# Performance work log

Measured on AMD Instinct MI355X. Metric: run time of the kernel, lower is better.

## Reference

```python
import jax, jax.numpy as jnp
import numpy as np

D_MODEL = 1024
NUM_HEADS = 16
D_K = D_MODEL // NUM_HEADS
B, S = 2, 2048


def setup_inputs() -> dict:
    key = jax.random.key(0)
    ks = jax.random.split(key, 13)
    s = 1.0 / np.sqrt(D_MODEL)
    inp = {
        "query": jax.random.normal(ks[0], (B, S, D_MODEL), jnp.float32),
        "key_": jax.random.normal(ks[1], (B, S, D_MODEL), jnp.float32),
        "value": jax.random.normal(ks[2], (B, S, D_MODEL), jnp.float32),
        "mask": jax.random.randint(ks[3], (B, 1, 1, S), 0, 2, jnp.int32),
        # torch nn.Linear convention: weight (out, in), y = x @ W.T + b
        "Wq": jax.random.uniform(ks[4], (D_MODEL, D_MODEL), jnp.float32, -s, s),
        "bq": jax.random.uniform(ks[5], (D_MODEL,), jnp.float32, -s, s),
        "Wk": jax.random.uniform(ks[6], (D_MODEL, D_MODEL), jnp.float32, -s, s),
        "bk": jax.random.uniform(ks[7], (D_MODEL,), jnp.float32, -s, s),
        "Wv": jax.random.uniform(ks[8], (D_MODEL, D_MODEL), jnp.float32, -s, s),
        "bv": jax.random.uniform(ks[9], (D_MODEL,), jnp.float32, -s, s),
        "Wo": jax.random.uniform(ks[10], (D_MODEL, D_MODEL), jnp.float32, -s, s),
        "bo": jax.random.uniform(ks[11], (D_MODEL,), jnp.float32, -s, s),
    }
    return inp


def _split_heads(x):
    b, s, _ = x.shape
    return x.reshape(b, s, NUM_HEADS, D_K).transpose(0, 2, 1, 3)  # (B,H,S,dk)


def reference(query, key_, value, mask, Wq, bq, Wk, bk, Wv, bv, Wo, bo):
    Q = _split_heads(query @ Wq.T + bq)
    K = _split_heads(key_ @ Wk.T + bk)
    V = _split_heads(value @ Wv.T + bv)
    scores = jnp.einsum("bhqd,bhkd->bhqk", Q, K) / np.sqrt(D_K).astype(np.float32)
    scores = jnp.where(mask == 0, -jnp.inf, scores)
    attn = jax.nn.softmax(scores, axis=-1)
    attn = jnp.nan_to_num(attn)  # fully-masked rows -> 0 (matches torch.nan_to_num)
    ctx = jnp.einsum("bhqk,bhkd->bhqd", attn, V)
    concat = ctx.transpose(0, 2, 1, 3).reshape(query.shape[0], -1, D_MODEL)
    out = concat @ Wo.T + bo  # dropout is identity in eval mode
    return out
```

## Files before the change

kernel.cpp:

```cpp
#include <hip/hip_runtime.h>
#include <math.h>

#define D_MODEL 1024
#define NUM_HEADS 16
#define DK 64
#define BATCH 2
#define SEQ 2048

using f32x4  = __attribute__((ext_vector_type(4))) float;
using f16x8  = __attribute__((ext_vector_type(8))) _Float16;

__device__ __forceinline__ void gl_lds16(const void* g, void* l) {
    __builtin_amdgcn_global_load_lds(
        (const __attribute__((address_space(1))) void*)g,
        (__attribute__((address_space(3))) void*)l, 16, 0, 0);
}

__global__ __launch_bounds__(256) void mask_scan_kernel(
    const int* __restrict__ mask, int* __restrict__ pos, int* __restrict__ nc)
{
    const int b = blockIdx.x;
    const int tid = threadIdx.x;
    __shared__ int sums[256];
    int v[8]; int cnt = 0;
    const int base = b * SEQ + tid * 8;
    #pragma unroll
    for (int e = 0; e < 8; ++e) { v[e] = (mask[base + e] != 0) ? 1 : 0; cnt += v[e]; }
    sums[tid] = cnt;
    __syncthreads();
    for (int off = 1; off < 256; off <<= 1) {
        int t = (tid >= off) ? sums[tid - off] : 0;
        __syncthreads();
        sums[tid] += t;
        __syncthreads();
    }
    int run = sums[tid] - cnt;
    #pragma unroll
    for (int e = 0; e < 8; ++e) { pos[base + e] = run; run += v[e]; }
    if (tid == 255) nc[b] = sums[255];
}

__global__ __launch_bounds__(256) void conv_all_kernel(
    const float* Wq, const float* Wk, const float* Wv, const float* Wo,
    const float* query, const float* key_, const float* value,
    _Float16* w2q, _Float16* w2k, _Float16* w2v, _Float16* w2o,
    _Float16* aq, _Float16* ak, _Float16* av,
    const int* __restrict__ mask, const int* __restrict__ pos)
{
    const int y = blockIdx.y;
    const float* src; _Float16* dst; int rows; bool compact = false;
    switch (y) {
        case 0: src = Wq;    dst = w2q; rows = 1024; break;
        case 1: src = Wk;    dst = w2k; rows = 1024; break;
        case 2: src = Wv;    dst = w2v; rows = 1024; break;
        case 3: src = Wo;    dst = w2o; rows = 1024; break;
        case 4: src = query; dst = aq;  rows = 4096; break;
        case 5: src = key_;  dst = ak;  rows = 4096; compact = true; break;
        default: src = value; dst = av; rows = 4096; compact = true; break;
    }
    const int id = blockIdx.x * 256 + threadIdx.x;
    if (id >= rows * 128) return;
    const int row = id >> 7;
    int drow = row;
    if (compact) {
        if (!mask[row]) return;
        drow = (row >> 11) * SEQ + pos[row];
    }
    const int s  = id & 127;
    const int g  = s >> 3, ss = s & 7;
    const int lb = ss ^ (drow & 7);

    const float* p = src + (size_t)row * 1024 + g * 64 + lb * 8;
    const float4 a = *(const float4*)p;
    const float4 bq = *(const float4*)(p + 4);
    f16x8 o;
    o[0] = (_Float16)a.x;  o[1] = (_Float16)a.y;
    o[2] = (_Float16)a.z;  o[3] = (_Float16)a.w;
    o[4] = (_Float16)bq.x; o[5] = (_Float16)bq.y;
    o[6] = (_Float16)bq.z; o[7] = (_Float16)bq.w;
    *(f16x8*)&dst[(size_t)drow * 1024 + s * 8] = o;
}

template <int MODE>
__global__ __launch_bounds__(256) void mfma_gemm_f16_kernel(
    const _Float16* __restrict__ A2, const _Float16* __restrict__ W2,
    const float* __restrict__ bias, float* __restrict__ Cf,
    _Float16* __restrict__ Ch, const int* __restrict__ ncArr)
{
    constexpr int KS = 1024;
    __shared__ f16x8 Asl[3][1024];
    __shared__ f16x8 Bsl[3][512];

    const int bm = blockIdx.x * 128, bn = blockIdx.y * 64;
    if (MODE == 2 || MODE == 3) {
        if ((bm & (SEQ - 1)) >= ncArr[bm >> 11]) return;
    }

    const int tid = threadIdx.x;
    const int wv = tid >> 6, ln = tid & 63;
    const int wm = wv >> 1, wn = wv & 1;
    const int x = ln & 15, y = ln >> 4;

    f32x4 acc[4][2] = {};

    const _Float16* Ab = A2 + (size_t)bm * KS;
    const _Float16* Bb = W2 + (size_t)bn * KS;
    const int srow = ln >> 3;
    const int scol = (ln & 7) * 8;

    auto stage = [&](int bufi, int kt) {
        #pragma unroll
        for (int c = 0; c < 4; ++c) {
            const int rowb = wv * 32 + c * 8;
            gl_lds16(Ab + (size_t)(rowb + srow) * KS + kt * 64 + scol,
                     &Asl[bufi][rowb << 3]);
        }
        #pragma unroll
        for (int c = 0; c < 2; ++c) {
            const int rowb = wv * 16 + c * 8;
            gl_lds16(Bb + (size_t)(rowb + srow) * KS + kt * 64 + scol,
                     &Bsl[bufi][rowb << 3]);
        }
    };

    stage(0, 0);
    stage(1, 1);

    int buf = 0, sbuf = 2;
    for (int kt = 0; kt < 16; ++kt) {
        if (kt < 15) asm volatile("s_waitcnt vmcnt(6)" ::: "memory");
        else         asm volatile("s_waitcnt vmcnt(0)" ::: "memory");
        __builtin_amdgcn_s_barrier();
        if (kt + 2 < 16) stage(sbuf, kt + 2);
        #pragma unroll
        for (int half = 0; half < 2; ++half) {
            f16x8 af[4], bfr[2];
            #pragma unroll
            for (int mf = 0; mf < 4; ++mf) {
                const int r = wm * 64 + mf * 16 + x;
                af[mf] = Asl[buf][(r << 3) | ((half * 4 + y) ^ (r & 7))];
            }
            #pragma unroll
            for (int nf = 0; nf < 2; ++nf) {
                const int r = wn * 32 + nf * 16 + x;
                bfr[nf] = Bsl[buf][(r << 3) | ((half * 4 + y) ^ (r & 7))];
            }
            #pragma unroll
            for (int mf = 0; mf < 4; ++mf)
                #pragma unroll
                for (int nf = 0; nf < 2; ++nf)
                    acc[mf][nf] = __builtin_amdgcn_mfma_f32_16x16x32_f16(
                        af[mf], bfr[nf], acc[mf][nf], 0, 0, 0);
        }
        buf  = (buf  == 2) ? 0 : buf  + 1;
        sbuf = (sbuf == 2) ? 0 : sbuf + 1;
    }

    #pragma unroll
    for (int nf = 0; nf < 2; ++nf) {
        const int n = bn + wn * 32 + nf * 16 + x;
        const float bv = bias[n];
        #pragma unroll
        for (int mf = 0; mf < 4; ++mf) {
            const int mbase = bm + wm * 64 + mf * 16 + y * 4;
            #pragma unroll
            for (int r = 0; r < 4; ++r) {
                const int m = mbase + r;
                const float v = acc[mf][nf][r] + bv;
                const int b = m >> 11, s = m & (SEQ - 1);
                const int hh = n >> 6, dd = n & 63;
                if (MODE == 0) {
                    Cf[(size_t)m * D_MODEL + n] = v;
                } else if (MODE == 1) {
                    const int blk = (dd >> 3) ^ (s & 7), i = dd & 7;
                    Ch[((size_t)((b * NUM_HEADS + hh) * SEQ + s)) * 64 +
                       blk * 8 + i] = (_Float16)(v * 0.125f);
                } else if (MODE == 2) {
                    if (s < ncArr[b]) {
                        const int blk = (dd >> 3) ^ (s & 7), i = dd & 7;
                        Ch[((size_t)((b * NUM_HEADS + hh) * SEQ + s)) * 64 +
                           blk * 8 + i] = (_Float16)v;
                    }
                } else {
                    if (s < ncArr[b]) {
                        const int tile = s >> 6, w = s & 63;
                        const int blk = (w >> 3) ^ (dd & 7), i = w & 7;
                        Ch[((size_t)((b * NUM_HEADS + hh) * DK + dd)) * SEQ +
                           tile * 64 + blk * 8 + i] = (_Float16)v;
                    }
                }
            }
        }
    }
}

__global__ __launch_bounds__(256, 4) void attn_mfma_kernel(
    const _Float16* __restrict__ Q2, const _Float16* __restrict__ K2,
    const _Float16* __restrict__ VT2, const int* __restrict__ ncArr,
    _Float16* __restrict__ ACT)
{
    __shared__ __align__(16) _Float16 SM[20480];

    const int tid = threadIdx.x;
    const int wave = tid >> 6, lane = tid & 63;
    const int lo4 = lane & 15, hi4 = lane >> 4;
    _Float16* Pw = SM + 16384 + wave * 1024;

    const int orig = blockIdx.x;
    const int swz = (orig & 7) * 128 + (orig >> 3);
    const int bh = swz >> 5, qblk = swz & 31;
    const int b = bh >> 4, h = bh & 15;

    const _Float16* Kb = K2 + (size_t)bh * SEQ * 64;
    const _Float16* Vb = VT2 + (size_t)bh * DK * SEQ;

    const int ncb = ncArr[b];
    const int ntiles = (ncb + 63) >> 6;

    const int qr = qblk * 64 + wave * 16 + lo4;
    const _Float16* Q2row = Q2 + (size_t)(bh * SEQ + qr) * 64;
    f16x8 qf[2];
    #pragma unroll
    for (int c = 0; c < 2; ++c)
        qf[c] = *(const f16x8*)&Q2row[(((c * 4 + hi4) ^ (qr & 7)) * 8)];

    auto stage_kv = [&](int base, int k0) {
        #pragma unroll
        for (int j = 0; j < 4; ++j) {
            const int g = j * 256 + wave * 64;
            const int gi = g + lane;
            const _Float16* src;
            if (gi < 512) {
                src = Kb + (size_t)(k0 + (gi >> 3)) * 64 + (gi & 7) * 8;
            } else {
                const int g2 = gi - 512;
                src = Vb + (size_t)(g2 >> 3) * SEQ + k0 + (g2 & 7) * 8;
            }
            gl_lds16(src, SM + base + (size_t)g * 8);
        }
    };

    f32x4 ctx[4] = {};
    float m = -INFINITY, l = 0.f;

    stage_kv(0, 0);
    for (int t = 0; t < ntiles; ++t) {
        if (t + 1 < ntiles) {
            stage_kv(((t + 1) & 1) * 8192, (t + 1) * 64);
            asm volatile("s_waitcnt vmcnt(4)" ::: "memory");
        } else {
            asm volatile("s_waitcnt vmcnt(0)" ::: "memory");
        }
        __builtin_amdgcn_s_barrier();

        const _Float16* Ks = SM + (t & 1) * 8192;
        const _Float16* VTs = Ks + 4096;
        const int k0 = t * 64;

        f32x4 sc[4];
        __builtin_amdgcn_s_setprio(1);
        #pragma unroll
        for (int kt = 0; kt < 4; ++kt) {
            f32x4 s = {0.f, 0.f, 0.f, 0.f};
            const int row = kt * 16 + lo4;
            const int rx = row & 7;
            #pragma unroll
            for (int c = 0; c < 2; ++c) {
                const f16x8 kf = *(f16x8*)&Ks[row * 64 + (((c * 4 + hi4) ^ rx) * 8)];
                s = __builtin_amdgcn_mfma_f32_16x16x32_f16(kf, qf[c], s, 0, 0, 0);
            }
            sc[kt] = s;
        }
        __builtin_amdgcn_s_setprio(0);

        float cmax = -1e30f;
        if (k0 + 64 <= ncb) {
            #pragma unroll
            for (int kt = 0; kt < 4; ++kt)
                #pragma unroll
                for (int r = 0; r < 4; ++r) cmax = fmaxf(cmax, sc[kt][r]);
        } else {
            #pragma unroll
            for (int kt = 0; kt < 4; ++kt)
                #pragma unroll
                for (int r = 0; r < 4; ++r) {
                    const int kidx = k0 + kt * 16 + hi4 * 4 + r;
                    const float sv = (kidx < ncb) ? sc[kt][r] : -1e30f;
                    sc[kt][r] = sv;
                    cmax = fmaxf(cmax, sv);
                }
        }
        cmax = fmaxf(cmax, __shfl_xor(cmax, 16));
        cmax = fmaxf(cmax, __shfl_xor(cmax, 32));

        const bool grow = __any(cmax > m);
        const float mold = m;
        const float mnew = grow ? fmaxf(m, cmax) : m;
        m = mnew;

        float ps = 0.f;
        #pragma unroll
        for (int kt = 0; kt < 4; ++kt) {
            const float pv0 = __expf(sc[kt][0] - mnew);
            const float pv1 = __expf(sc[kt][1] - mnew);
            const float pv2 = __expf(sc[kt][2] - mnew);
            const float pv3 = __expf(sc[kt][3] - mnew);
            ps += (pv0 + pv1) + (pv2 + pv3);
            union { _Float16 hh[2]; unsigned u; } pk0, pk1;
            pk0.hh[0] = (_Float16)pv0; pk0.hh[1] = (_Float16)pv1;
            pk1.hh[0] = (_Float16)pv2; pk1.hh[1] = (_Float16)pv3;
            const int blk16 = (kt * 2 + (hi4 >> 1)) ^ (lo4 & 7);
            unsigned* dst = (unsigned*)&Pw[lo4 * 64 + blk16 * 8 + (hi4 & 1) * 4];
            dst[0] = pk0.u; dst[1] = pk1.u;
        }
        ps += __shfl_xor(ps, 16);
        ps += __shfl_xor(ps, 32);

        if (grow) {
            const float e1 = __expf(mold - mnew);
            l = l * e1 + ps;
            #pragma unroll
            for (int dt = 0; dt < 4; ++dt)
                #pragma unroll
                for (int r = 0; r < 4; ++r) ctx[dt][r] *= e1;
        } else {
            l += ps;
        }

        __builtin_amdgcn_s_setprio(1);
        #pragma unroll
        for (int c = 0; c < 2; ++c) {
            const f16x8 pf = *(f16x8*)&Pw[lo4 * 64 + (((c * 4 + hi4) ^ (lo4 & 7)) * 8)];
            #pragma unroll
            for (int dt = 0; dt < 4; ++dt) {
                const int row = dt * 16 + lo4;
                const f16x8 vf =
                    *(f16x8*)&VTs[row * 64 + (((c * 4 + hi4) ^ (row & 7)) * 8)];
                ctx[dt] = __builtin_amdgcn_mfma_f32_16x16x32_f16(vf, pf, ctx[dt], 0, 0, 0);
            }
        }
        __builtin_amdgcn_s_setprio(0);

        __builtin_amdgcn_s_barrier();
    }

    __syncthreads();
    const float inv = (l > 0.f) ? (1.f / l) : 0.f;
    float* OutL = (float*)SM;
    #pragma unroll
    for (int dt = 0; dt < 4; ++dt)
        #pragma unroll
        for (int r = 0; r < 4; ++r)
            OutL[(wave * 16 + lo4) * 68 + dt * 16 + hi4 * 4 + r] = ctx[dt][r] * inv;
    __syncthreads();
    {
        const int row = tid >> 2, cb = (tid & 3) * 16;
        const int mrow = b * SEQ + qblk * 64 + row;
        _Float16* arow = ACT + (size_t)mrow * 1024;
        #pragma unroll
        for (int u = 0; u < 2; ++u) {
            const int lb = (cb >> 3) + u;
            const int ss = lb ^ (mrow & 7);
            f16x8 hv;
            #pragma unroll
            for (int i = 0; i < 8; ++i)
                hv[i] = (_Float16)OutL[row * 68 + cb + u * 8 + i];
            *(f16x8*)&arow[h * 64 + ss * 8] = hv;
        }
    }
}

template <int SPLIT>
__global__ __launch_bounds__(256) void gemm_bias_kernel(
    const float* __restrict__ A, const float* __restrict__ W,
    const float* __restrict__ bias, float* __restrict__ C,
    int M, int N, int K)
{
    constexpr int TILE = 64, KT = 16;
    __shared__ float As[KT][TILE + 4];
    __shared__ float Ws[KT][TILE + 4];
    const int tid = threadIdx.x;
    const int tx = tid & 15, ty = tid >> 4;
    const int bm = blockIdx.x * TILE, bn = blockIdx.y * TILE;
    const int lrow = tid >> 2, lk4 = (tid & 3) << 2;
    float acc[4][4] = {{0.f}};
    for (int k0 = 0; k0 < K; k0 += KT) {
        const float4 a4 = *(const float4*)&A[(size_t)(bm + lrow) * K + k0 + lk4];
        const float4 w4 = *(const float4*)&W[(size_t)(bn + lrow) * K + k0 + lk4];
        __syncthreads();
        As[lk4 + 0][lrow] = a4.x; As[lk4 + 1][lrow] = a4.y;
        As[lk4 + 2][lrow] = a4.z; As[lk4 + 3][lrow] = a4.w;
        Ws[lk4 + 0][lrow] = w4.x; Ws[lk4 + 1][lrow] = w4.y;
        Ws[lk4 + 2][lrow] = w4.z; Ws[lk4 + 3][lrow] = w4.w;
        __syncthreads();
        #pragma unroll
        for (int kk = 0; kk < KT; ++kk) {
            const float4 av = *(const float4*)&As[kk][ty << 2];
            const float4 wv = *(const float4*)&Ws[kk][tx << 2];
            acc[0][0] += av.x * wv.x; acc[0][1] += av.x * wv.y; acc[0][2] += av.x * wv.z; acc[0][3] += av.x * wv.w;
            acc[1][0] += av.y * wv.x; acc[1][1] += av.y * wv.y; acc[1][2] += av.y * wv.z; acc[1][3] += av.y * wv.w;
            acc[2][0] += av.z * wv.x; acc[2][1] += av.z * wv.y; acc[2][2] += av.z * wv.z; acc[2][3] += av.z * wv.w;
            acc[3][0] += av.w * wv.x; acc[3][1] += av.w * wv.y; acc[3][2] += av.w * wv.z; acc[3][3] += av.w * wv.w;
        }
    }
    const float4 bb = *(const float4*)&bias[bn + (tx << 2)];
    #pragma unroll
    for (int i = 0; i < 4; ++i) {
        const int row = bm + (ty << 2) + i;
        float4 o;
        o.x = acc[i][0] + bb.x; o.y = acc[i][1] + bb.y;
        o.z = acc[i][2] + bb.z; o.w = acc[i][3] + bb.w;
        if (SPLIT) {
            const int b = row >> 11, s = row & (SEQ - 1), hh = bn >> 6;
            *(float4*)&C[((size_t)((b * NUM_HEADS + hh) * SEQ + s)) * DK + (tx << 2)] = o;
        } else {
            *(float4*)&C[(size_t)row * N + bn + (tx << 2)] = o;
        }
    }
}

__global__ __launch_bounds__(256, 2) void attn_fp32_kernel(
    const float* __restrict__ Q, const float* __restrict__ K,
    const float* __restrict__ V, const int* __restrict__ mask,
    float* __restrict__ OUT)
{
    const int qb = blockIdx.x, h = blockIdx.y, b = blockIdx.z;
    const int wave = threadIdx.x >> 6, lane = threadIdx.x & 63;
    const int tid = threadIdx.x;
    const int bh = b * NUM_HEADS + h;
    const float* Qb = Q + (size_t)bh * SEQ * DK;
    const float* Kb = K + (size_t)bh * SEQ * DK;
    const float* Vb = V + (size_t)bh * SEQ * DK;
    const int* mb = mask + b * SEQ;
    __shared__ float Ks[64][68];
    __shared__ float Vs[64][68];
    const int row = qb * 256 + wave * 64 + lane;
    float q[DK], ctx[DK];
    #pragma unroll
    for (int d4 = 0; d4 < 16; ++d4) {
        const float4 t = *(const float4*)&Qb[(size_t)row * DK + 4 * d4];
        q[4*d4] = t.x; q[4*d4+1] = t.y; q[4*d4+2] = t.z; q[4*d4+3] = t.w;
        ctx[4*d4] = 0.f; ctx[4*d4+1] = 0.f; ctx[4*d4+2] = 0.f; ctx[4*d4+3] = 0.f;
    }
    float m = -INFINITY, l = 0.f;
    for (int t = 0; t < SEQ / 64; ++t) {
        const int k0 = t * 64;
        const float* Kt = Kb + (size_t)k0 * DK;
        const float* Vt = Vb + (size_t)k0 * DK;
        __syncthreads();
        #pragma unroll
        for (int i = 0; i < 4; ++i) {
            const int f4 = i * 256 + tid;
            const int r = f4 >> 4, c = (f4 & 15) << 2;
            *(float4*)&Ks[r][c] = *(const float4*)&Kt[4 * f4];
            *(float4*)&Vs[r][c] = *(const float4*)&Vt[4 * f4];
        }
        __syncthreads();
        const unsigned long long mbits = __ballot(mb[k0 + lane] != 0);
        if (mbits == 0ULL) continue;
        for (int c0 = 0; c0 < 64; c0 += 16) {
            const unsigned bits = (unsigned)((mbits >> c0) & 0xFFFFULL);
            if (!bits) continue;
            float sc[16];
            #pragma unroll
            for (int j = 0; j < 16; ++j) {
                if (!((bits >> j) & 1u)) { sc[j] = -INFINITY; continue; }
                float a0 = 0.f, a1 = 0.f, a2 = 0.f, a3 = 0.f;
                #pragma unroll
                for (int d4 = 0; d4 < 16; ++d4) {
                    const float4 kv = *(const float4*)&Ks[c0 + j][4 * d4];
                    a0 += q[4*d4] * kv.x; a1 += q[4*d4+1] * kv.y;
                    a2 += q[4*d4+2] * kv.z; a3 += q[4*d4+3] * kv.w;
                }
                sc[j] = ((a0 + a1) + (a2 + a3)) * 0.125f;
            }
            float cmax = sc[0];
            #pragma unroll
            for (int j = 1; j < 16; ++j) cmax = fmaxf(cmax, sc[j]);
            if (cmax > m) {
                const float scale = __expf(m - cmax);
                l *= scale;
                #pragma unroll
                for (int d = 0; d < DK; ++d) ctx[d] *= scale;
                m = cmax;
            }
            #pragma unroll
            for (int j = 0; j < 16; ++j) {
                if (!((bits >> j) & 1u)) continue;
                const float p = __expf(sc[j] - m);
                l += p;
                #pragma unroll
                for (int d4 = 0; d4 < 16; ++d4) {
                    const float4 vv = *(const float4*)&Vs[c0 + j][4 * d4];
                    ctx[4*d4] += p * vv.x; ctx[4*d4+1] += p * vv.y;
                    ctx[4*d4+2] += p * vv.z; ctx[4*d4+3] += p * vv.w;
                }
            }
        }
    }
    const float inv = (l > 0.f) ? (1.f / l) : 0.f;
    float* dst = OUT + ((size_t)(b * SEQ + row)) * D_MODEL + h * DK;
    #pragma unroll
    for (int d4 = 0; d4 < 16; ++d4) {
        float4 o;
        o.x = ctx[4*d4] * inv; o.y = ctx[4*d4+1] * inv;
        o.z = ctx[4*d4+2] * inv; o.w = ctx[4*d4+3] * inv;
        *(float4*)&dst[4 * d4] = o;
    }
}

extern "C" void kernel_launch(void* const* d_in, const int* in_sizes, int n_in,
                              void* d_out, int out_size, void* d_ws, size_t ws_size,
                              hipStream_t stream)
{
    const float* query = (const float*)d_in[0];
    const float* key_  = (const float*)d_in[1];
    const float* value = (const float*)d_in[2];
    const int*   mask  = (const int*)d_in[3];
    const float* Wq = (const float*)d_in[4];
    const float* bq = (const float*)d_in[5];
    const float* Wk = (const float*)d_in[6];
    const float* bk = (const float*)d_in[7];
    const float* Wv = (const float*)d_in[8];
    const float* bv = (const float*)d_in[9];
    const float* Wo = (const float*)d_in[10];
    const float* bo = (const float*)d_in[11];
    float* out = (float*)d_out;

    const int M = BATCH * SEQ;
    const size_t ACT_B = (size_t)M * 1024 * 2;
    const size_t W_B   = (size_t)D_MODEL * 1024 * 2;
    const size_t K2_B  = (size_t)32 * SEQ * 64 * 2;
    const size_t VT2_B = (size_t)32 * DK * SEQ * 2;
    const size_t Q2_B  = K2_B;
    const size_t POS_B = (size_t)BATCH * SEQ * 4 + 256;

    char* base = (char*)d_ws;
    _Float16* actQh = (_Float16*)(base);
    _Float16* actKh = (_Float16*)(base + ACT_B);
    _Float16* actVh = (_Float16*)(base + 2 * ACT_B);
    _Float16* actO  = (_Float16*)(base + 3 * ACT_B);
    _Float16* w2qh  = (_Float16*)(base + 4 * ACT_B);
    _Float16* w2kh  = (_Float16*)((char*)w2qh + W_B);
    _Float16* w2vh  = (_Float16*)((char*)w2kh + W_B);
    _Float16* w2oh  = (_Float16*)((char*)w2vh + W_B);
    _Float16* k2    = (_Float16*)((char*)w2oh + W_B);
    _Float16* vt2   = (_Float16*)((char*)k2 + K2_B);
    _Float16* q2    = (_Float16*)((char*)vt2 + VT2_B);
    int* posArr = (int*)((char*)q2 + Q2_B);
    int* ncArr  = posArr + BATCH * SEQ;
    const size_t need = 4 * ACT_B + 4 * W_B + K2_B + VT2_B + Q2_B + POS_B;

    if (ws_size >= need) {
        mask_scan_kernel<<<BATCH, 256, 0, stream>>>(mask, posArr, ncArr);

        conv_all_kernel<<<dim3(2048, 7), 256, 0, stream>>>(
            Wq, Wk, Wv, Wo, query, key_, value,
            w2qh, w2kh, w2vh, w2oh, actQh, actKh, actVh, mask, posArr);

        dim3 ggrid(M / 128, D_MODEL / 64);
        mfma_gemm_f16_kernel<2><<<ggrid, 256, 0, stream>>>(
            actKh, w2kh, bk, nullptr, k2, ncArr);
        mfma_gemm_f16_kernel<3><<<ggrid, 256, 0, stream>>>(
            actVh, w2vh, bv, nullptr, vt2, ncArr);
        mfma_gemm_f16_kernel<1><<<ggrid, 256, 0, stream>>>(
            actQh, w2qh, bq, nullptr, q2, ncArr);

        attn_mfma_kernel<<<1024, 256, 0, stream>>>(q2, k2, vt2, ncArr, actO);

        mfma_gemm_f16_kernel<0><<<ggrid, 256, 0, stream>>>(
            actO, w2oh, bo, out, nullptr, ncArr);
    } else {
        float* q_ws = (float*)(base);
        float* k_ws = (float*)(base + (size_t)M * D_MODEL * 4);
        float* v_ws = (float*)(base + 2 * (size_t)M * D_MODEL * 4);
        float* c_ws = (float*)(base + 3 * (size_t)M * D_MODEL * 4);
        dim3 ggrid(M / 64, D_MODEL / 64);
        gemm_bias_kernel<1><<<ggrid, 256, 0, stream>>>(query, Wq, bq, q_ws, M, D_MODEL, D_MODEL);
        gemm_bias_kernel<1><<<ggrid, 256, 0, stream>>>(key_,  Wk, bk, k_ws, M, D_MODEL, D_MODEL);
        gemm_bias_kernel<1><<<ggrid, 256, 0, stream>>>(value, Wv, bv, v_ws, M, D_MODEL, D_MODEL);
        dim3 agrid(SEQ / 256, NUM_HEADS, BATCH);
        attn_fp32_kernel<<<agrid, 256, 0, stream>>>(q_ws, k_ws, v_ws, mask, c_ws);
        gemm_bias_kernel<0><<<ggrid, 256, 0, stream>>>(c_ws, Wo, bo, out, M, D_MODEL, D_MODEL);
    }
}
```

Measured before the change: 130.7 us.

## Process 128 query rows per attention block to reuse staged K/V tiles

Each wave now handles two 16-row query fragments instead of one, so every block covers 128 query rows and the grid halves from 1024 to 512 blocks. Each K/V tile staged into LDS is reused for twice as many queries, which halves global K/V traffic and the barrier count per query. In exchange, register pressure rises (two context accumulators and two sets of softmax state), the occupancy hint in launch_bounds is dropped, and fewer blocks are available to fill the GPU's compute units.

```diff
diff --git a/kernel.cpp b/kernel.cpp
--- a/kernel.cpp
+++ b/kernel.cpp
@@ -194,7 +194,7 @@
     }
 }
 
-__global__ __launch_bounds__(256, 4) void attn_mfma_kernel(
+__global__ __launch_bounds__(256) void attn_mfma_kernel(
     const _Float16* __restrict__ Q2, const _Float16* __restrict__ K2,
     const _Float16* __restrict__ VT2, const int* __restrict__ ncArr,
     _Float16* __restrict__ ACT)
@@ -207,8 +207,8 @@
     _Float16* Pw = SM + 16384 + wave * 1024;
 
     const int orig = blockIdx.x;
-    const int swz = (orig & 7) * 128 + (orig >> 3);
-    const int bh = swz >> 5, qblk = swz & 31;
+    const int swz = (orig & 7) * 64 + (orig >> 3);
+    const int bh = swz >> 4, qblk = swz & 15;
     const int b = bh >> 4, h = bh & 15;
 
     const _Float16* Kb = K2 + (size_t)bh * SEQ * 64;
@@ -217,12 +217,15 @@
     const int ncb = ncArr[b];
     const int ntiles = (ncb + 63) >> 6;
 
-    const int qr = qblk * 64 + wave * 16 + lo4;
-    const _Float16* Q2row = Q2 + (size_t)(bh * SEQ + qr) * 64;
-    f16x8 qf[2];
-    #pragma unroll
-    for (int c = 0; c < 2; ++c)
-        qf[c] = *(const f16x8*)&Q2row[(((c * 4 + hi4) ^ (qr & 7)) * 8)];
+    f16x8 qf[2][2];
+    #pragma unroll
+    for (int f = 0; f < 2; ++f) {
+        const int qr = qblk * 128 + wave * 32 + f * 16 + lo4;
+        const _Float16* Q2row = Q2 + (size_t)(bh * SEQ + qr) * 64;
+        #pragma unroll
+        for (int c = 0; c < 2; ++c)
+            qf[f][c] = *(const f16x8*)&Q2row[(((c * 4 + hi4) ^ (qr & 7)) * 8)];
+    }
 
     auto stage_kv = [&](int base, int k0) {
         #pragma unroll
@@ -240,8 +243,8 @@
         }
     };
 
-    f32x4 ctx[4] = {};
-    float m = -INFINITY, l = 0.f;
+    f32x4 ctx[2][4] = {};
+    float m[2] = {-INFINITY, -INFINITY}, l[2] = {0.f, 0.f};
 
     stage_kv(0, 0);
     for (int t = 0; t < ntiles; ++t) {
@@ -256,116 +259,125 @@
         const _Float16* Ks = SM + (t & 1) * 8192;
         const _Float16* VTs = Ks + 4096;
         const int k0 = t * 64;
-
-        f32x4 sc[4];
-        __builtin_amdgcn_s_setprio(1);
-        #pragma unroll
-        for (int kt = 0; kt < 4; ++kt) {
-            f32x4 s = {0.f, 0.f, 0.f, 0.f};
-            const int row = kt * 16 + lo4;
-            const int rx = row & 7;
+        const bool fulltile = (k0 + 64 <= ncb);
+
+        #pragma unroll
+        for (int f = 0; f < 2; ++f) {
+            f32x4 sc[4];
+            __builtin_amdgcn_s_setprio(1);
+            #pragma unroll
+            for (int kt = 0; kt < 4; ++kt) {
+                f32x4 s = {0.f, 0.f, 0.f, 0.f};
+                const int row = kt * 16 + lo4;
+                const int rx = row & 7;
+                #pragma unroll
+                for (int c = 0; c < 2; ++c) {
+                    const f16x8 kf = *(f16x8*)&Ks[row * 64 + (((c * 4 + hi4) ^ rx) * 8)];
+                    s = __builtin_amdgcn_mfma_f32_16x16x32_f16(kf, qf[f][c], s, 0, 0, 0);
+                }
+                sc[kt] = s;
+            }
+            __builtin_amdgcn_s_setprio(0);
+
+            float cmax = -1e30f;
+            if (fulltile) {
+                #pragma unroll
+                for (int kt = 0; kt < 4; ++kt)
+                    #pragma unroll
+                    for (int r = 0; r < 4; ++r) cmax = fmaxf(cmax, sc[kt][r]);
+            } else {
+                #pragma unroll
+                for (int kt = 0; kt < 4; ++kt)
+                    #pragma unroll
+                    for (int r = 0; r < 4; ++r) {
+                        const int kidx = k0 + kt * 16 + hi4 * 4 + r;
+                        const float sv = (kidx < ncb) ? sc[kt][r] : -1e30f;
+                        sc[kt][r] = sv;
+                        cmax = fmaxf(cmax, sv);
+                    }
+            }
+            cmax = fmaxf(cmax, __shfl_xor(cmax, 16));
+            cmax = fmaxf(cmax, __shfl_xor(cmax, 32));
+
+            const bool grow = __any(cmax > m[f]);
+            const float mold = m[f];
+            const float mnew = grow ? fmaxf(m[f], cmax) : m[f];
+            m[f] = mnew;
+
+            float ps = 0.f;
+            #pragma unroll
+            for (int kt = 0; kt < 4; ++kt) {
+                const float pv0 = __expf(sc[kt][0] - mnew);
+                const float pv1 = __expf(sc[kt][1] - mnew);
+                const float pv2 = __expf(sc[kt][2] - mnew);
+                const float pv3 = __expf(sc[kt][3] - mnew);
+                ps += (pv0 + pv1) + (pv2 + pv3);
+                union { _Float16 hh[2]; unsigned u; } pk0, pk1;
+                pk0.hh[0] = (_Float16)pv0; pk0.hh[1] = (_Float16)pv1;
+                pk1.hh[0] = (_Float16)pv2; pk1.hh[1] = (_Float16)pv3;
+                const int blk16 = (kt * 2 + (hi4 >> 1)) ^ (lo4 & 7);
+                unsigned* dst = (unsigned*)&Pw[lo4 * 64 + blk16 * 8 + (hi4 & 1) * 4];
+                dst[0] = pk0.u; dst[1] = pk1.u;
+            }
+            ps += __shfl_xor(ps, 16);
+            ps += __shfl_xor(ps, 32);
+
+            if (grow) {
+                const float e1 = __expf(mold - mnew);
+                l[f] = l[f] * e1 + ps;
+                #pragma unroll
+                for (int dt = 0; dt < 4; ++dt)
+                    #pragma unroll
+                    for (int r = 0; r < 4; ++r) ctx[f][dt][r] *= e1;
+            } else {
+                l[f] += ps;
+            }
+
+            __builtin_amdgcn_s_setprio(1);
             #pragma unroll
             for (int c = 0; c < 2; ++c) {
-                const f16x8 kf = *(f16x8*)&Ks[row * 64 + (((c * 4 + hi4) ^ rx) * 8)];
-                s = __builtin_amdgcn_mfma_f32_16x16x32_f16(kf, qf[c], s, 0, 0, 0);
-            }
-            sc[kt] = s;
-        }
-        __builtin_amdgcn_s_setprio(0);
-
-        float cmax = -1e30f;
-        if (k0 + 64 <= ncb) {
-            #pragma unroll
-            for (int kt = 0; kt < 4; ++kt)
-                #pragma unroll
-                for (int r = 0; r < 4; ++r) cmax = fmaxf(cmax, sc[kt][r]);
-        } else {
-            #pragma unroll
-            for (int kt = 0; kt < 4; ++kt)
-                #pragma unroll
-                for (int r = 0; r < 4; ++r) {
-                    const int kidx = k0 + kt * 16 + hi4 * 4 + r;
-                    const float sv = (kidx < ncb) ? sc[kt][r] : -1e30f;
-                    sc[kt][r] = sv;
-                    cmax = fmaxf(cmax, sv);
+                const f16x8 pf = *(f16x8*)&Pw[lo4 * 64 + (((c * 4 + hi4) ^ (lo4 & 7)) * 8)];
+                #pragma unroll
+                for (int dt = 0; dt < 4; ++dt) {
+                    const int row = dt * 16 + lo4;
+                    const f16x8 vf =
+                        *(f16x8*)&VTs[row * 64 + (((c * 4 + hi4) ^ (row & 7)) * 8)];
+                    ctx[f][dt] = __builtin_amdgcn_mfma_f32_16x16x32_f16(vf, pf, ctx[f][dt], 0, 0, 0);
                 }
-        }
-        cmax = fmaxf(cmax, __shfl_xor(cmax, 16));
-        cmax = fmaxf(cmax, __shfl_xor(cmax, 32));
-
-        const bool grow = __any(cmax > m);
-        const float mold = m;
-        const float mnew = grow ? fmaxf(m, cmax) : m;
-        m = mnew;
-
-        float ps = 0.f;
-        #pragma unroll
-        for (int kt = 0; kt < 4; ++kt) {
-            const float pv0 = __expf(sc[kt][0] - mnew);
-            const float pv1 = __expf(sc[kt][1] - mnew);
-            const float pv2 = __expf(sc[kt][2] - mnew);
-            const float pv3 = __expf(sc[kt][3] - mnew);
-            ps += (pv0 + pv1) + (pv2 + pv3);
-            union { _Float16 hh[2]; unsigned u; } pk0, pk1;
-            pk0.hh[0] = (_Float16)pv0; pk0.hh[1] = (_Float16)pv1;
-            pk1.hh[0] = (_Float16)pv2; pk1.hh[1] = (_Float16)pv3;
-            const int blk16 = (kt * 2 + (hi4 >> 1)) ^ (lo4 & 7);
-            unsigned* dst = (unsigned*)&Pw[lo4 * 64 + blk16 * 8 + (hi4 & 1) * 4];
-            dst[0] = pk0.u; dst[1] = pk1.u;
-        }
-        ps += __shfl_xor(ps, 16);
-        ps += __shfl_xor(ps, 32);
-
-        if (grow) {
-            const float e1 = __expf(mold - mnew);
-            l = l * e1 + ps;
-            #pragma unroll
-            for (int dt = 0; dt < 4; ++dt)
-                #pragma unroll
-                for (int r = 0; r < 4; ++r) ctx[dt][r] *= e1;
-        } else {
-            l += ps;
-        }
-
-        __builtin_amdgcn_s_setprio(1);
-        #pragma unroll
-        for (int c = 0; c < 2; ++c) {
-            const f16x8 pf = *(f16x8*)&Pw[lo4 * 64 + (((c * 4 + hi4) ^ (lo4 & 7)) * 8)];
-            #pragma unroll
-            for (int dt = 0; dt < 4; ++dt) {
-                const int row = dt * 16 + lo4;
-                const f16x8 vf =
-                    *(f16x8*)&VTs[row * 64 + (((c * 4 + hi4) ^ (row & 7)) * 8)];
-                ctx[dt] = __builtin_amdgcn_mfma_f32_16x16x32_f16(vf, pf, ctx[dt], 0, 0, 0);
-            }
-        }
-        __builtin_amdgcn_s_setprio(0);
+            }
+            __builtin_amdgcn_s_setprio(0);
+        }
 
         __builtin_amdgcn_s_barrier();
     }
 
-    __syncthreads();
-    const float inv = (l > 0.f) ? (1.f / l) : 0.f;
-    float* OutL = (float*)SM;
-    #pragma unroll
-    for (int dt = 0; dt < 4; ++dt)
-        #pragma unroll
-        for (int r = 0; r < 4; ++r)
-            OutL[(wave * 16 + lo4) * 68 + dt * 16 + hi4 * 4 + r] = ctx[dt][r] * inv;
-    __syncthreads();
-    {
-        const int row = tid >> 2, cb = (tid & 3) * 16;
-        const int mrow = b * SEQ + qblk * 64 + row;
-        _Float16* arow = ACT + (size_t)mrow * 1024;
-        #pragma unroll
-        for (int u = 0; u < 2; ++u) {
-            const int lb = (cb >> 3) + u;
-            const int ss = lb ^ (mrow & 7);
-            f16x8 hv;
-            #pragma unroll
-            for (int i = 0; i < 8; ++i)
-                hv[i] = (_Float16)OutL[row * 68 + cb + u * 8 + i];
-            *(f16x8*)&arow[h * 64 + ss * 8] = hv;
+    #pragma unroll
+    for (int f = 0; f < 2; ++f) {
+        __syncthreads();
+        const float inv = (l[f] > 0.f) ? (1.f / l[f]) : 0.f;
+        float* OutL = (float*)SM;
+        #pragma unroll
+        for (int dt = 0; dt < 4; ++dt)
+            #pragma unroll
+            for (int r = 0; r < 4; ++r)
+                OutL[(wave * 16 + lo4) * 68 + dt * 16 + hi4 * 4 + r] =
+                    ctx[f][dt][r] * inv;
+        __syncthreads();
+        {
+            const int row = tid >> 2, cb = (tid & 3) * 16;
+            const int mrow = b * SEQ + qblk * 128 + (row >> 4) * 32 + f * 16
+                           + (row & 15);
+            _Float16* arow = ACT + (size_t)mrow * 1024;
+            #pragma unroll
+            for (int u = 0; u < 2; ++u) {
+                const int lb = (cb >> 3) + u;
+                const int ss = lb ^ (mrow & 7);
+                f16x8 hv;
+                #pragma unroll
+                for (int i = 0; i < 8; ++i)
+                    hv[i] = (_Float16)OutL[row * 68 + cb + u * 8 + i];
+                *(f16x8*)&arow[h * 64 + ss * 8] = hv;
+            }
         }
     }
 }
@@ -566,7 +578,7 @@
         mfma_gemm_f16_kernel<1><<<ggrid, 256, 0, stream>>>(
             actQh, w2qh, bq, nullptr, q2, ncArr);
 
-        attn_mfma_kernel<<<1024, 256, 0, stream>>>(q2, k2, vt2, ncArr, actO);
+        attn_mfma_kernel<<<512, 256, 0, stream>>>(q2, k2, vt2, ncArr, actO);
 
         mfma_gemm_f16_kernel<0><<<ggrid, 256, 0, stream>>>(
             actO, w2oh, bo, out, nullptr, ncArr);
```

After: 138.4 us. +5.9%, slower.
